# Performance work log

Hardware: AMD Instinct MI355X
Metric: run time of the kernel (lower is better)

The kernel has to match this reference:

```python
import jax, jax.numpy as jnp
import numpy as np

B, S, E = 8, 2048, 128
DECAY = 1.2
LN_EPS = 1e-3  # keras LayerNormalization default epsilon


def setup_inputs() -> dict:
    key = jax.random.key(0)
    k1, k2, k3, k4 = jax.random.split(key, 4)
    return {
        "x": jax.random.normal(k1, (B, S, E), dtype=jnp.float32),
        "dense_w": jax.random.normal(k2, (E, E), dtype=jnp.float32) * 0.02,
        "dense_b": jnp.zeros((E,), dtype=jnp.float32),
        "concept_map": jax.random.normal(k3, (E, E, E), dtype=jnp.float32) * 0.02,
        "ln_gamma": jnp.ones((E,), dtype=jnp.float32),
        "ln_beta": jnp.zeros((E,), dtype=jnp.float32),
    }


def reference(x, dense_w, dense_b, concept_map, ln_gamma, ln_beta):
    # Dense projection
    h = x @ dense_w + dense_b  # (B, S, E)
    b, s, e = h.shape

    # Decayed prefix-sum recurrence: s_i = (s_{i-1} + h_{i-1}) / 1.2, s_0 = 0
    def step(carry, xt):
        new = (carry + xt) / DECAY
        return new, new

    h_t = jnp.swapaxes(h, 0, 1)  # (S, B, E)
    _, s_tail = jax.lax.scan(step, jnp.zeros((b, e), h.dtype), h_t[:-1])
    s_seq = jnp.concatenate([jnp.zeros((1, b, e), h.dtype), s_tail], axis=0)
    s_seq = jnp.swapaxes(s_seq, 0, 1)  # (B, S, E)

    # result[b,s,c] = sum_{a,p} h[b,s,a] * s_seq[b,s,p] * W[c,a,p]
    # (original code materializes (B,S,E,E,E); this is the fused contraction)
    out = jnp.einsum("bsa,bsp,cap->bsc", h, s_seq, concept_map)

    r = out + h
    # LayerNormalization over the last axis
    mean = jnp.mean(r, axis=-1, keepdims=True)
    var = jnp.var(r, axis=-1, keepdims=True)
    r = (r - mean) * jax.lax.rsqrt(var + LN_EPS) * ln_gamma + ln_beta
    # Dropout is identity at inference
    return r
```

## Files before the change

### kernel.cpp

```cpp
#include <hip/hip_runtime.h>
#include <hip/hip_bf16.h>
#include <math.h>

#define E_DIM 128
#define S_LEN 2048
#define B_N   8
#define BS    (B_N * S_LEN)
#define CHUNK 64
#define NCHUNK (S_LEN / CHUNK)

typedef unsigned short u16;
typedef _Float16 f16;
typedef _Float16 f16x2 __attribute__((ext_vector_type(2)));
typedef _Float16 f16x8 __attribute__((ext_vector_type(8)));
typedef float    f32x16 __attribute__((ext_vector_type(16)));

__global__ __launch_bounds__(256) void k_pre(const float* __restrict__ x,
                                             const float* __restrict__ dw,
                                             const float* __restrict__ db,
                                             const float* __restrict__ cm,
                                             float* __restrict__ hout,
                                             u16* __restrict__ wb) {
    if (blockIdx.x < 1024) {
        int t = blockIdx.x * 256 + threadIdx.x;
        int qs = t & 15, c = (t >> 4) & 127, a = t >> 11;
        const float* src = cm + (((long)(c << 7) + a) << 7) + ((qs ^ (c & 15)) << 3);
        float4 v0 = ((const float4*)src)[0];
        float4 v1 = ((const float4*)src)[1];
        union { f16 f[8]; uint4 v; } o;
        o.f[0] = (f16)v0.x; o.f[1] = (f16)v0.y; o.f[2] = (f16)v0.z; o.f[3] = (f16)v0.w;
        o.f[4] = (f16)v1.x; o.f[5] = (f16)v1.y; o.f[6] = (f16)v1.z; o.f[7] = (f16)v1.w;
        ((uint4*)wb)[t] = o.v;
        return;
    }
    __shared__ float Wl[E_DIM * E_DIM];
    const int t = threadIdx.x;
    const long r0 = (long)(blockIdx.x - 1024) * 64;

    float4* Wl4 = (float4*)Wl;
    const float4* w4 = (const float4*)dw;
#pragma unroll
    for (int i = 0; i < 16; ++i) Wl4[t + 256 * i] = w4[t + 256 * i];
    __syncthreads();

    const int cq = t & 31;
    const int rg = t >> 5;
    float4 bb = ((const float4*)db)[cq];
    float acc[8][4];
#pragma unroll
    for (int i = 0; i < 8; ++i) {
        acc[i][0] = bb.x; acc[i][1] = bb.y; acc[i][2] = bb.z; acc[i][3] = bb.w;
    }
#pragma unroll 4
    for (int k = 0; k < E_DIM; ++k) {
        float4 wv = Wl4[k * 32 + cq];
#pragma unroll
        for (int i = 0; i < 8; ++i) {
            float xv = x[(r0 + rg * 8 + i) * E_DIM + k];
            acc[i][0] += xv * wv.x;
            acc[i][1] += xv * wv.y;
            acc[i][2] += xv * wv.z;
            acc[i][3] += xv * wv.w;
        }
    }
    float4* h4 = (float4*)(hout + r0 * E_DIM);
#pragma unroll
    for (int i = 0; i < 8; ++i) {
        float4 o;
        o.x = acc[i][0]; o.y = acc[i][1]; o.z = acc[i][2]; o.w = acc[i][3];
        h4[(rg * 8 + i) * 32 + cq] = o;
    }
}

__global__ __launch_bounds__(128) void k_scan(const float* __restrict__ h,
                                              u16* __restrict__ sb16,
                                              float* __restrict__ fc,
                                              u16* __restrict__ hT) {
    const int b = blockIdx.x >> 5;
    const int j = blockIdx.x & 31;
    const int e = threadIdx.x;
    const float inv_d = (float)(1.0 / 1.2);
    const int pos0 = b * S_LEN + j * CHUNK;
    long base = (long)pos0 * E_DIM + e;
    float carry = 0.f;
    union { u16 u[8]; uint4 v; } hb;
#pragma unroll 1
    for (int i0 = 0; i0 < CHUNK; i0 += 8) {
#pragma unroll
        for (int k = 0; k < 8; ++k) {
            float hv = h[base + (long)(i0 + k) * E_DIM];
            union { f16 f; u16 u; } cu; cu.f = (f16)carry;
            sb16[base + (long)(i0 + k) * E_DIM] = cu.u;
            union { f16 f; u16 u; } hu; hu.f = (f16)hv;
            hb.u[k] = hu.u;
            carry = (carry + hv) * inv_d;
        }
        *(uint4*)&hT[(size_t)e * BS + pos0 + i0] = hb.v;
    }
    fc[(b * NCHUNK + j) * E_DIM + e] = carry;
}

__global__ __launch_bounds__(512, 2) void k_main(const u16* __restrict__ hT,
                                                 const u16* __restrict__ sb16,
                                                 const float* __restrict__ fc,
                                                 const u16* __restrict__ wb,
                                                 float* __restrict__ out,
                                                 float dm64) {
    __shared__ u16 Wl[4][16384];
    __shared__ u16 h16[32 * 256];
    __shared__ float carr[4][E_DIM];
    const int t = threadIdx.x;
    const int w = t >> 6, l = t & 63;
    const int l31 = l & 31, hi = l >> 5;
    const int mb = blockIdx.x >> 2, r = blockIdx.x & 3;
    const int rbp = w >> 1;
    const int ntp = w & 1;
    const int row_base = mb * 256;

    const u16* wbK = wb + (size_t)(r * 32) * 16384;

#define STAGE(buf, sl) {                                                          \
    const u16* gsrc = wbK + (size_t)(sl) * 16384 + t * 8;                         \
    _Pragma("unroll")                                                             \
    for (int i = 0; i < 4; ++i)                                                   \
        __builtin_amdgcn_global_load_lds(                                         \
            (const __attribute__((address_space(1))) void*)(gsrc + i * 4096),     \
            (__attribute__((address_space(3))) void*)&Wl[buf][t * 8 + i * 4096],  \
            16, 0, 0); }

    STAGE(0, 0);
    STAGE(1, 1);

    const int bb = row_base >> 11;
    const int j0 = (row_base >> 6) & 31;
    {
        const int ch = t >> 7, e = t & 127;
        float c = 0.f;
        for (int jj = 0; jj < j0 + ch; ++jj)
            c = fc[(bb * NCHUNK + jj) * E_DIM + e] + c * dm64;
        carr[ch][e] = c;
    }
    {
        const int al = t >> 4, rl0 = (t & 15) * 16;
        const u16* src = hT + (size_t)(r * 32 + al) * BS + row_base + rl0;
        uint4 v0 = ((const uint4*)src)[0];
        uint4 v1 = ((const uint4*)src)[1];
        *(uint4*)&h16[al * 256 + rl0] = v0;
        *(uint4*)&h16[al * 256 + rl0 + 8] = v1;
    }
    __syncthreads();

    const float L2D = 0.26303440583379383f;
    f16x2 s2[2][32];
#pragma unroll
    for (int rb = 0; rb < 2; ++rb) {
        const int row = row_base + rbp * 64 + rb * 32 + l31;
        const float f = exp2f(-L2D * (float)(row & 63));
        const uint4* sp = (const uint4*)(sb16 + (size_t)row * E_DIM + hi * 8);
#pragma unroll
        for (int ks = 0; ks < 8; ++ks) {
            union { uint4 u; u16 us[8]; } uu; uu.u = sp[ks * 2];
            const float* cp = &carr[rbp][ks * 16 + hi * 8];
#pragma unroll
            for (int q = 0; q < 4; ++q) {
                union { f16 f; u16 u; } a0; a0.u = uu.us[2 * q];
                union { f16 f; u16 u; } a1; a1.u = uu.us[2 * q + 1];
                f16x2 pr;
                pr.x = (f16)((float)a0.f + cp[2 * q] * f);
                pr.y = (f16)((float)a1.f + cp[2 * q + 1] * f);
                s2[rb][ks * 4 + q] = pr;
            }
        }
    }

    f32x16 acc[2][2];
#pragma unroll
    for (int rb = 0; rb < 2; ++rb)
#pragma unroll
        for (int nt = 0; nt < 2; ++nt)
#pragma unroll
            for (int g = 0; g < 16; ++g) acc[rb][nt][g] = 0.f;

    const int sxb = l31 & 15;
    const int wcoff = (ntp * 64 + l31) * E_DIM;
    const int hoff0 = rbp * 64 + l31;

#pragma unroll 1
    for (int sl = 0; sl < 32; ++sl) {
        if (sl < 30) { asm volatile("s_waitcnt vmcnt(4)" ::: "memory"); }
        else         { asm volatile("s_waitcnt vmcnt(0)" ::: "memory"); }
        __builtin_amdgcn_s_barrier();
        if (sl < 30) { STAGE((sl + 2) & 3, sl + 2); }

        u16 hv0 = h16[sl * 256 + hoff0];
        u16 hv1 = h16[sl * 256 + hoff0 + 32];
        union { u16 u[2]; f16x2 v; } hu0, hu1;
        hu0.u[0] = hv0; hu0.u[1] = hv0;
        hu1.u[0] = hv1; hu1.u[1] = hv1;

        const u16* Wc = &Wl[sl & 3][wcoff];
        __builtin_amdgcn_s_setprio(1);
#pragma unroll
        for (int ks = 0; ks < 8; ++ks) {
            const int sx = ((ks << 1) + hi) ^ sxb;
            f16x8 b0 = *(const f16x8*)(Wc + sx * 8);
            f16x8 b1 = *(const f16x8*)(Wc + 32 * E_DIM + sx * 8);
            union { f16x2 h2[4]; f16x8 v; } a0, a1;
#pragma unroll
            for (int q = 0; q < 4; ++q) {
                a0.h2[q] = hu0.v * s2[0][ks * 4 + q];
                a1.h2[q] = hu1.v * s2[1][ks * 4 + q];
            }
            acc[0][0] = __builtin_amdgcn_mfma_f32_32x32x16_f16(a0.v, b0, acc[0][0], 0, 0, 0);
            acc[0][1] = __builtin_amdgcn_mfma_f32_32x32x16_f16(a0.v, b1, acc[0][1], 0, 0, 0);
            acc[1][0] = __builtin_amdgcn_mfma_f32_32x32x16_f16(a1.v, b0, acc[1][0], 0, 0, 0);
            acc[1][1] = __builtin_amdgcn_mfma_f32_32x32x16_f16(a1.v, b1, acc[1][1], 0, 0, 0);
        }
        __builtin_amdgcn_s_setprio(0);
    }
#undef STAGE

#pragma unroll
    for (int rb = 0; rb < 2; ++rb)
#pragma unroll
        for (int nt = 0; nt < 2; ++nt)
#pragma unroll
            for (int g = 0; g < 16; ++g) {
                int rowl = (g & 3) + 8 * (g >> 2) + 4 * hi;
                long row = (long)row_base + rbp * 64 + rb * 32 + rowl;
                int col = ntp * 64 + nt * 32 + l31;
                unsafeAtomicAdd(&out[row * E_DIM + col], acc[rb][nt][g]);
            }
}

__global__ __launch_bounds__(256) void k_ln(float* __restrict__ out,
                                            const float* __restrict__ h,
                                            const float* __restrict__ gamma,
                                            const float* __restrict__ beta) {
    const int t = threadIdx.x;
    const int l32 = t & 31, rl = t >> 5;
    const long row = (long)blockIdx.x * 8 + rl;
    float4 v  = ((const float4*)out)[row * 32 + l32];
    float4 hv = ((const float4*)h)[row * 32 + l32];
    v.x += hv.x; v.y += hv.y; v.z += hv.z; v.w += hv.w;
    float ls = v.x + v.y + v.z + v.w;
    float lq = v.x * v.x + v.y * v.y + v.z * v.z + v.w * v.w;
#pragma unroll
    for (int m = 1; m < 32; m <<= 1) {
        ls += __shfl_xor(ls, m, 64);
        lq += __shfl_xor(lq, m, 64);
    }
    float mean = ls * (1.f / 128.f);
    float var  = lq * (1.f / 128.f) - mean * mean;
    float inv  = rsqrtf(var + 1e-3f);
    float4 g = ((const float4*)gamma)[l32];
    float4 b = ((const float4*)beta)[l32];
    float4 o;
    o.x = (v.x - mean) * inv * g.x + b.x;
    o.y = (v.y - mean) * inv * g.y + b.y;
    o.z = (v.z - mean) * inv * g.z + b.z;
    o.w = (v.w - mean) * inv * g.w + b.w;
    ((float4*)out)[row * 32 + l32] = o;
}

extern "C" void kernel_launch(void* const* d_in, const int* in_sizes, int n_in,
                              void* d_out, int out_size, void* d_ws, size_t ws_size,
                              hipStream_t stream) {
    const float* x     = (const float*)d_in[0];
    const float* dw    = (const float*)d_in[1];
    const float* db    = (const float*)d_in[2];
    const float* cm    = (const float*)d_in[3];
    const float* gamma = (const float*)d_in[4];
    const float* beta  = (const float*)d_in[5];
    float* outp = (float*)d_out;

    float* ws = (float*)d_ws;
    float* h    = ws;
    float* fc   = ws + (size_t)BS * E_DIM;
    u16*   wb   = (u16*)(fc + B_N * NCHUNK * E_DIM);
    u16*   hT   = wb + (size_t)2097152;
    u16*   sb16 = hT + (size_t)BS * E_DIM;

    float dm64 = (float)pow(1.2, -64.0);

    hipMemsetAsync(d_out, 0, (size_t)BS * E_DIM * sizeof(float), stream);
    k_pre <<<dim3(1280), dim3(256), 0, stream>>>(x, dw, db, cm, h, wb);
    k_scan<<<dim3(B_N * NCHUNK), dim3(128), 0, stream>>>(h, sb16, fc, hT);
    k_main<<<dim3(256), dim3(512), 0, stream>>>(hT, sb16, fc, wb, outp, dm64);
    k_ln  <<<dim3(BS / 8), dim3(256), 0, stream>>>(outp, h, gamma, beta);
}
```

Before: 129.0 us.

## Interleave weight staging with MFMA in barrier-fenced quarter phases

Splits each 32-slice iteration into four phases. Each phase reads two k-steps of B operands from LDS, issues one quarter of the next-next slice's global-to-LDS copy, then runs eight MFMAs between barriers with raised priority. The goal is to spread load issue across the compute and to get a ping-pong schedule between waves. In exchange it adds eight barriers per slice instead of one. It also reads LDS for the first phase before any barrier, so it may read data that other waves have not finished staging.

```diff
diff --git a/kernel.cpp b/kernel.cpp
--- a/kernel.cpp
+++ b/kernel.cpp
@@ -128,6 +128,13 @@
             (__attribute__((address_space(3))) void*)&Wl[buf][t * 8 + i * 4096],  \
             16, 0, 0); }
 
+#define STAGE_Q(buf, sl, q) {                                                     \
+    const u16* gsrc = wbK + (size_t)(sl) * 16384 + (q) * 4096 + t * 8;            \
+    __builtin_amdgcn_global_load_lds(                                             \
+        (const __attribute__((address_space(1))) void*)gsrc,                      \
+        (__attribute__((address_space(3))) void*)&Wl[buf][(q) * 4096 + t * 8],    \
+        16, 0, 0); }
+
     STAGE(0, 0);
     STAGE(1, 1);
 
@@ -189,8 +196,6 @@
     for (int sl = 0; sl < 32; ++sl) {
         if (sl < 30) { asm volatile("s_waitcnt vmcnt(4)" ::: "memory"); }
         else         { asm volatile("s_waitcnt vmcnt(0)" ::: "memory"); }
-        __builtin_amdgcn_s_barrier();
-        if (sl < 30) { STAGE((sl + 2) & 3, sl + 2); }
 
         u16 hv0 = h16[sl * 256 + hoff0];
         u16 hv1 = h16[sl * 256 + hoff0 + 32];
@@ -199,26 +204,45 @@
         hu1.u[0] = hv1; hu1.u[1] = hv1;
 
         const u16* Wc = &Wl[sl & 3][wcoff];
-        __builtin_amdgcn_s_setprio(1);
-#pragma unroll
-        for (int ks = 0; ks < 8; ++ks) {
-            const int sx = ((ks << 1) + hi) ^ sxb;
-            f16x8 b0 = *(const f16x8*)(Wc + sx * 8);
-            f16x8 b1 = *(const f16x8*)(Wc + 32 * E_DIM + sx * 8);
-            union { f16x2 h2[4]; f16x8 v; } a0, a1;
+
+#pragma unroll
+        for (int p = 0; p < 4; ++p) {
+            const int ks0 = 2 * p, ks1 = 2 * p + 1;
+            const int sx0 = ((ks0 << 1) + hi) ^ sxb;
+            const int sx1 = ((ks1 << 1) + hi) ^ sxb;
+            f16x8 b00 = *(const f16x8*)(Wc + sx0 * 8);
+            f16x8 b01 = *(const f16x8*)(Wc + 32 * E_DIM + sx0 * 8);
+            f16x8 b10 = *(const f16x8*)(Wc + sx1 * 8);
+            f16x8 b11 = *(const f16x8*)(Wc + 32 * E_DIM + sx1 * 8);
+            if (sl < 30) { STAGE_Q((sl + 2) & 3, sl + 2, p); }
+
+            __builtin_amdgcn_s_barrier();
+            asm volatile("s_waitcnt lgkmcnt(0)" ::: "memory");
+            __builtin_amdgcn_sched_barrier(0);
+
+            __builtin_amdgcn_s_setprio(1);
+            union { f16x2 h2[4]; f16x8 v; } a00, a10, a01, a11;
 #pragma unroll
             for (int q = 0; q < 4; ++q) {
-                a0.h2[q] = hu0.v * s2[0][ks * 4 + q];
-                a1.h2[q] = hu1.v * s2[1][ks * 4 + q];
+                a00.h2[q] = hu0.v * s2[0][ks0 * 4 + q];
+                a10.h2[q] = hu1.v * s2[1][ks0 * 4 + q];
+                a01.h2[q] = hu0.v * s2[0][ks1 * 4 + q];
+                a11.h2[q] = hu1.v * s2[1][ks1 * 4 + q];
             }
-            acc[0][0] = __builtin_amdgcn_mfma_f32_32x32x16_f16(a0.v, b0, acc[0][0], 0, 0, 0);
-            acc[0][1] = __builtin_amdgcn_mfma_f32_32x32x16_f16(a0.v, b1, acc[0][1], 0, 0, 0);
-            acc[1][0] = __builtin_amdgcn_mfma_f32_32x32x16_f16(a1.v, b0, acc[1][0], 0, 0, 0);
-            acc[1][1] = __builtin_amdgcn_mfma_f32_32x32x16_f16(a1.v, b1, acc[1][1], 0, 0, 0);
+            acc[0][0] = __builtin_amdgcn_mfma_f32_32x32x16_f16(a00.v, b00, acc[0][0], 0, 0, 0);
+            acc[0][1] = __builtin_amdgcn_mfma_f32_32x32x16_f16(a00.v, b01, acc[0][1], 0, 0, 0);
+            acc[1][0] = __builtin_amdgcn_mfma_f32_32x32x16_f16(a10.v, b00, acc[1][0], 0, 0, 0);
+            acc[1][1] = __builtin_amdgcn_mfma_f32_32x32x16_f16(a10.v, b01, acc[1][1], 0, 0, 0);
+            acc[0][0] = __builtin_amdgcn_mfma_f32_32x32x16_f16(a01.v, b10, acc[0][0], 0, 0, 0);
+            acc[0][1] = __builtin_amdgcn_mfma_f32_32x32x16_f16(a01.v, b11, acc[0][1], 0, 0, 0);
+            acc[1][0] = __builtin_amdgcn_mfma_f32_32x32x16_f16(a11.v, b10, acc[1][0], 0, 0, 0);
+            acc[1][1] = __builtin_amdgcn_mfma_f32_32x32x16_f16(a11.v, b11, acc[1][1], 0, 0, 0);
+            __builtin_amdgcn_s_setprio(0);
+            __builtin_amdgcn_s_barrier();
         }
-        __builtin_amdgcn_s_setprio(0);
     }
 #undef STAGE
+#undef STAGE_Q
 
 #pragma unroll
     for (int rb = 0; rb < 2; ++rb)
```

Result: no change. 131.1 us (+1.7%).
